# Kernel optimization log

Hardware: AMD Instinct MI355X
Metric: run time of the kernel (lower is better)

The kernel has to match this reference:

```python
import jax, jax.numpy as jnp
import numpy as np

B, L = 16, 1024
D_MODEL, D_STATE, N_LAYERS = 256, 16, 2
FRAME_DIM, N_FRAMES, N_ACT = 115, 4, 19
GNN_H, GNN_K, ACT_EMB, GRID, N_PLAYERS = 32, 6, 16, 5, 22


def _ln(x, g, b, eps=1e-5):
    m = x.mean(-1, keepdims=True)
    v = ((x - m) ** 2).mean(-1, keepdims=True)
    return (x - m) / jnp.sqrt(v + eps) * g + b


def _kan(x, g, b, Wsp, Wbase, bias, beta):
    # x: [N, FRAME_DIM]
    grid = jnp.linspace(-1.0, 1.0, GRID)
    x = _ln(x, g, b)
    bta = jnp.clip(beta, 0.5, 6.0)
    basis = jnp.exp(-((x[..., None] - grid) ** 2) * bta)  # [N, I, G]
    # original: einsum('bdig,oid->bod').sum(-1) with basis dim d==1 broadcast
    # == sum over i, g (basis) and d (spline grid axis)
    spline = jnp.einsum('big,oid->bo', basis, Wsp)
    base = x @ Wbase.T
    return base + spline + bias


def _graph(fc, fp):
    # fc, fp: [N, 115] current / previous frame
    Bn = fc.shape[0]
    ball = fc[:, :2]
    lp = fc[:, 3:25].reshape(Bn, 11, 2)
    rp = fc[:, 25:47].reshape(Bn, 11, 2)
    lpp = fp[:, 3:25].reshape(Bn, 11, 2)
    rpp = fp[:, 25:47].reshape(Bn, 11, 2)
    pos = jnp.concatenate([lp, rp], 1)           # [N, 22, 2]
    posp = jnp.concatenate([lpp, rpp], 1)
    vel = pos - posp
    team = jnp.concatenate([jnp.zeros((Bn, 11, 1)), jnp.ones((Bn, 11, 1))], 1)
    bd = jnp.sqrt(((pos - ball[:, None, :]) ** 2).sum(-1, keepdims=True))
    prox = jnp.exp(-bd * 2)
    lc = lp.mean(1, keepdims=True)
    rc = rp.mean(1, keepdims=True)
    tc = jnp.concatenate([jnp.broadcast_to(lc, (Bn, 11, 2)),
                          jnp.broadcast_to(rc, (Bn, 11, 2))], 1)
    nodes = jnp.concatenate([pos, vel, team, prox, pos - tc], -1)  # [N, 22, 8]
    eye = jnp.eye(N_PLAYERS)
    d = jnp.sqrt(((pos[:, :, None, :] - pos[:, None, :, :]) ** 2).sum(-1)) + eye * 1e6
    _, idx = jax.lax.top_k(-d, GNN_K)
    adj = jax.nn.one_hot(idx, N_PLAYERS).sum(-2)
    adj = jnp.minimum(adj + eye, 1.0)
    adj = adj / jnp.clip(adj.sum(-1, keepdims=True), 1.0, None)
    # the torch model computes the graph under no_grad
    return jax.lax.stop_gradient(nodes), jax.lax.stop_gradient(adj)


def _s6(x, h0, lng, lnb, Win, Wdt, bdt, Alog, WB, WC, Dp, Wout):
    Bn, Ln, Dm = x.shape
    h0 = h0.reshape(Bn, Dm, D_STATE)
    xn = _ln(x, lng, lnb)
    xz = xn @ Win.T
    x_in, z = jnp.split(xz, 2, axis=-1)
    dt = jax.nn.softplus(x_in @ Wdt.T + bdt)     # [B, L, D]
    A = -jnp.exp(Alog)                            # [D, N]
    Bt = x_in @ WB.T                              # [B, L, N]
    Ct = x_in @ WC.T

    def step(h, inp):
        dt_t, x_t, B_t, C_t = inp                 # [B,D],[B,D],[B,N],[B,N]
        dA = jnp.exp(dt_t[:, :, None] * A)        # [B, D, N]
        h = dA * h + (dt_t * x_t)[:, :, None] * B_t[:, None, :]
        y = (h * C_t[:, None, :]).sum(-1)         # [B, D]
        return h, y

    hL, ys = jax.lax.scan(step, h0, (dt.swapaxes(0, 1), x_in.swapaxes(0, 1),
                                     Bt.swapaxes(0, 1), Ct.swapaxes(0, 1)))
    y = ys.swapaxes(0, 1)
    ssm = y * jax.nn.silu(z) + x_in * Dp
    return x + ssm @ Wout.T, hL.reshape(Bn, -1)


def setup_inputs() -> dict:
    key = jax.random.key(0)
    ks = iter(jax.random.split(key, 80))

    def nrm(shape, s=0.05):
        return jax.random.normal(next(ks), shape, dtype=jnp.float32) * s

    inp = {}
    inp['obs'] = jax.random.normal(next(ks), (B, L, N_FRAMES, FRAME_DIM), dtype=jnp.float32)
    inp['prev_actions'] = jax.random.randint(next(ks), (B, L), 0, N_ACT)
    inp['h0_0'] = jnp.zeros((B, D_MODEL * D_STATE), jnp.float32)
    inp['h0_1'] = jnp.zeros((B, D_MODEL * D_STATE), jnp.float32)
    inp['kan_ln_g'] = jnp.ones((FRAME_DIM,), jnp.float32)
    inp['kan_ln_b'] = jnp.zeros((FRAME_DIM,), jnp.float32)
    inp['kan_spline'] = nrm((D_MODEL, FRAME_DIM, GRID), 0.1)
    inp['kan_scale'] = jnp.ones((D_MODEL, FRAME_DIM), jnp.float32)
    inp['kan_bias'] = jnp.zeros((D_MODEL,), jnp.float32)
    inp['kan_beta'] = jnp.full((1,), 2.0, jnp.float32)
    inp['fn_g'] = jnp.ones((D_MODEL,), jnp.float32)
    inp['fn_b'] = jnp.zeros((D_MODEL,), jnp.float32)
    inp['gnn_W'] = nrm((GNN_H, 8))
    inp['edge_w'] = jnp.full((1,), 0.5, jnp.float32)
    inp['act_emb'] = nrm((N_ACT, ACT_EMB), 1.0)
    inp['W_ip'] = nrm((D_MODEL, D_MODEL + GNN_H + ACT_EMB))
    inp['b_ip'] = jnp.zeros((D_MODEL,), jnp.float32)
    for i in range(N_LAYERS):
        p = 'm%d_' % i
        inp[p + 'lng'] = jnp.ones((D_MODEL,), jnp.float32)
        inp[p + 'lnb'] = jnp.zeros((D_MODEL,), jnp.float32)
        inp[p + 'Win'] = nrm((2 * D_MODEL, D_MODEL))
        inp[p + 'Wdt'] = nrm((D_MODEL, D_MODEL))
        inp[p + 'bdt'] = jnp.zeros((D_MODEL,), jnp.float32)
        inp[p + 'Alog'] = jax.random.uniform(next(ks), (D_MODEL, D_STATE),
                                             minval=-3.0, maxval=-1.0, dtype=jnp.float32)
        inp[p + 'WB'] = nrm((D_STATE, D_MODEL))
        inp[p + 'WC'] = nrm((D_STATE, D_MODEL))
        inp[p + 'D'] = jnp.ones((D_MODEL,), jnp.float32)
        inp[p + 'Wout'] = nrm((D_MODEL, D_MODEL))
    inp['fl_g'] = jnp.ones((D_MODEL,), jnp.float32)
    inp['fl_b'] = jnp.zeros((D_MODEL,), jnp.float32)
    inp['pW1'] = nrm((128, D_MODEL)); inp['pb1'] = jnp.zeros((128,), jnp.float32)
    inp['pW2'] = nrm((N_ACT, 128)); inp['pb2'] = jnp.zeros((N_ACT,), jnp.float32)
    inp['vW1'] = nrm((64, D_MODEL)); inp['vb1'] = jnp.zeros((64,), jnp.float32)
    inp['vW2'] = nrm((1, 64)); inp['vb2'] = jnp.zeros((1,), jnp.float32)
    return inp


def reference(obs, prev_actions, h0_0, h0_1,
              kan_ln_g, kan_ln_b, kan_spline, kan_scale, kan_bias, kan_beta,
              fn_g, fn_b, gnn_W, edge_w, act_emb, W_ip, b_ip,
              m0_lng, m0_lnb, m0_Win, m0_Wdt, m0_bdt, m0_Alog, m0_WB, m0_WC, m0_D, m0_Wout,
              m1_lng, m1_lnb, m1_Win, m1_Wdt, m1_bdt, m1_Alog, m1_WB, m1_WC, m1_D, m1_Wout,
              fl_g, fl_b, pW1, pb1, pW2, pb2, vW1, vb1, vW2, vb2):
    BL = B * L
    # frame encoder (KAN) over all frames of all timesteps
    flat = obs.reshape(BL * N_FRAMES, FRAME_DIM)
    fe = _kan(flat, kan_ln_g, kan_ln_b, kan_spline, kan_scale, kan_bias, kan_beta)
    fe = jax.nn.relu(_ln(fe.reshape(BL, N_FRAMES, D_MODEL), fn_g, fn_b))
    feat = fe.mean(1)                                   # [BL, D]
    # GNN on last two frames
    fc = obs[:, :, -1, :].reshape(BL, FRAME_DIM)
    fp = obs[:, :, -2, :].reshape(BL, FRAME_DIM)
    nodes, adj = _graph(fc, fp)
    gx = nodes @ gnn_W.T                                # [BL, 22, H]
    agg = jnp.einsum('bij,bjd->bid', adj, gx)
    gx = gx * (1 - edge_w) + agg * edge_w
    gemb = gx.mean(1)                                   # [BL, H]
    aemb = act_emb[prev_actions].reshape(BL, ACT_EMB)
    x = jnp.concatenate([feat, gemb, aemb], -1) @ W_ip.T + b_ip
    x = x.reshape(B, L, D_MODEL)
    x, h1 = _s6(x, h0_0, m0_lng, m0_lnb, m0_Win, m0_Wdt, m0_bdt, m0_Alog, m0_WB, m0_WC, m0_D, m0_Wout)
    x, h2 = _s6(x, h0_1, m1_lng, m1_lnb, m1_Win, m1_Wdt, m1_bdt, m1_Alog, m1_WB, m1_WC, m1_D, m1_Wout)
    x = _ln(x, fl_g, fl_b)
    logits = jax.nn.relu(x @ pW1.T + pb1) @ pW2.T + pb2   # [B, L, N_ACT]
    value = (jax.nn.relu(x @ vW1.T + vb1) @ vW2.T + vb2)[..., 0]  # [B, L]
    return logits, value, h1, h2
```

## Files before the change

### kernel.cpp

```cpp
#include <hip/hip_runtime.h>
#include <math.h>

#define BB   16
#define LL   1024
#define BLR  (BB*LL)
#define DM   256
#define DS   16
#define FD   115
#define NF   4
#define NACTN 19
#define GH   32
#define GKN  6
#define AEM  16
#define NP   22
#define CATD 304
#define CATP 320
#define KKANP 256
#define KREALK 230
#define NC   16
#define CL   (LL/NC)
#define TT   16
#define LDK  40
#define XZW  800


typedef __attribute__((ext_vector_type(8))) short bf16x8;
typedef __attribute__((ext_vector_type(4))) float f32x4;

__device__ inline unsigned short f2bf(float f) {
    unsigned int u = __float_as_uint(f);
    u += 0x7fff + ((u >> 16) & 1);
    return (unsigned short)(u >> 16);
}
__device__ inline unsigned int f2bf2(float lo, float hi) {
    return (unsigned int)f2bf(lo) | ((unsigned int)f2bf(hi) << 16);
}
__device__ inline size_t swz(int row, int k) {
    return (size_t)(row >> 4)*4096 + (k >> 5)*512 + ((k >> 3) & 3)*128
         + (row & 15)*8 + (k & 7);
}

template<int NFRAG>
__global__ __launch_bounds__(256) void bgemm(
    const unsigned short* __restrict__ A, const unsigned short* __restrict__ W,
    const float* __restrict__ bias, float* __restrict__ C,
    int ldc, int act, int accum)
{
    const int tid = threadIdx.x;
    const int wid = tid >> 6, lane = tid & 63;
    const int wr = wid >> 1, wc = wid & 1;
    const int g = lane >> 4, r16 = lane & 15;
    const int bm = blockIdx.x * 64;
    const int bn = blockIdx.y * (NFRAG * 32);

    f32x4 acc[2][NFRAG] = {};
    const unsigned short* abase = A + ((size_t)(bm >> 4) + wr*2)*4096 + g*128 + r16*8;
    const unsigned short* wbase = W + ((size_t)(bn >> 4) + wc*NFRAG)*4096 + g*128 + r16*8;
    #pragma unroll
    for (int kk = 0; kk < 8; ++kk) {
        bf16x8 a0 = *(const bf16x8*)(abase + kk*512);
        bf16x8 a1 = *(const bf16x8*)(abase + 4096 + kk*512);
        bf16x8 bfr[NFRAG];
        #pragma unroll
        for (int ni = 0; ni < NFRAG; ++ni)
            bfr[ni] = *(const bf16x8*)(wbase + (size_t)ni*4096 + kk*512);
        #pragma unroll
        for (int ni = 0; ni < NFRAG; ++ni) {
            acc[0][ni] = __builtin_amdgcn_mfma_f32_16x16x32_bf16(a0, bfr[ni], acc[0][ni], 0,0,0);
            acc[1][ni] = __builtin_amdgcn_mfma_f32_16x16x32_bf16(a1, bfr[ni], acc[1][ni], 0,0,0);
        }
    }
    #pragma unroll
    for (int mi = 0; mi < 2; ++mi) {
        #pragma unroll
        for (int j = 0; j < 4; ++j) {
            int row = bm + wr*32 + mi*16 + g*4 + j;
            float* crow = C + (size_t)row * ldc;
            #pragma unroll
            for (int ni = 0; ni < NFRAG; ++ni) {
                int col = bn + wc*(NFRAG*16) + ni*16 + r16;
                float v = acc[mi][ni][j];
                if (act == 3) {
                    if (col >= 512 && col < 768) {
                        v += bias[col - 512];
                        v = fmaxf(v, 0.f) + __logf(1.f + __expf(-fabsf(v)));
                    }
                } else {
                    if (bias) v += bias[col];
                    if (act == 1) v = fmaxf(v, 0.f);
                }
                if (accum) v += crow[col];
                crow[col] = v;
            }
        }
    }
}

__global__ __launch_bounds__(256) void mfma_gemm(
    const float* __restrict__ A, const unsigned short* __restrict__ W,
    const float* __restrict__ bias, float* __restrict__ C,
    int N, int Kp, int Kreal, int lda, int ldc, int act, int accum)
{
    __shared__ __align__(16) unsigned short As[128*LDK];
    __shared__ __align__(16) unsigned short Ws[128*LDK];
    const int tid = threadIdx.x;
    const int bm = blockIdx.x * 128;
    const int bn = blockIdx.y * 128;
    const int wid = tid >> 6, lane = tid & 63;
    const int wr = wid >> 1, wc = wid & 1;
    const int g = lane >> 4, r16 = lane & 15;
    const int srow = tid >> 1;
    const int shalf = (tid & 1) * 16;

    f32x4 acc[4][4] = {};
    for (int k0 = 0; k0 < Kp; k0 += 32) {
        uint4 alo = make_uint4(0u,0u,0u,0u), ahi = make_uint4(0u,0u,0u,0u);
        if (k0 + shalf < Kreal) {
            const float* ap = A + (size_t)(bm + srow) * lda + k0 + shalf;
            float4 a0 = *(const float4*)(ap);
            float4 a1 = *(const float4*)(ap + 4);
            float4 a2 = *(const float4*)(ap + 8);
            float4 a3 = *(const float4*)(ap + 12);
            alo = make_uint4(f2bf2(a0.x,a0.y), f2bf2(a0.z,a0.w),
                             f2bf2(a1.x,a1.y), f2bf2(a1.z,a1.w));
            ahi = make_uint4(f2bf2(a2.x,a2.y), f2bf2(a2.z,a2.w),
                             f2bf2(a3.x,a3.y), f2bf2(a3.z,a3.w));
        }
        unsigned short* ad = &As[srow*LDK + shalf];
        *(uint4*)(ad)     = alo;
        *(uint4*)(ad + 8) = ahi;
        int n = bn + srow;
        uint4 wv0 = make_uint4(0u,0u,0u,0u), wv1 = make_uint4(0u,0u,0u,0u);
        if (n < N) {
            const unsigned short* wp = W + (size_t)n * Kp + k0 + shalf;
            wv0 = ((const uint4*)wp)[0];
            wv1 = ((const uint4*)wp)[1];
        }
        unsigned short* wd = &Ws[srow*LDK + shalf];
        *(uint4*)(wd)     = wv0;
        *(uint4*)(wd + 8) = wv1;
        __syncthreads();

        bf16x8 af[4], bfr[4];
        #pragma unroll
        for (int mi = 0; mi < 4; ++mi)
            af[mi] = *reinterpret_cast<const bf16x8*>(&As[(wr*64 + mi*16 + r16)*LDK + g*8]);
        #pragma unroll
        for (int ni = 0; ni < 4; ++ni)
            bfr[ni] = *reinterpret_cast<const bf16x8*>(&Ws[(wc*64 + ni*16 + r16)*LDK + g*8]);
        #pragma unroll
        for (int mi = 0; mi < 4; ++mi)
            #pragma unroll
            for (int ni = 0; ni < 4; ++ni)
                acc[mi][ni] = __builtin_amdgcn_mfma_f32_16x16x32_bf16(
                    af[mi], bfr[ni], acc[mi][ni], 0, 0, 0);
        __syncthreads();
    }
    #pragma unroll
    for (int mi = 0; mi < 4; ++mi) {
        #pragma unroll
        for (int j = 0; j < 4; ++j) {
            int row = bm + wr*64 + mi*16 + g*4 + j;
            float* crow = C + (size_t)row * ldc;
            #pragma unroll
            for (int ni = 0; ni < 4; ++ni) {
                int col = bn + wc*64 + ni*16 + r16;
                if (col < N) {
                    float v = acc[mi][ni][j];
                    if (bias) v += bias[col];
                    if (act == 1) v = fmaxf(v, 0.f);
                    if (accum) v += crow[col];
                    crow[col] = v;
                }
            }
        }
    }
}

__global__ __launch_bounds__(256) void kan_statgen(
    const float* __restrict__ obs, const float* __restrict__ lng,
    const float* __restrict__ lnb, const float* __restrict__ betap,
    unsigned short* __restrict__ AG)
{
    int row = blockIdx.x * 4 + (threadIdx.x >> 6);
    int l = threadIdx.x & 63;
    const float beta = fminf(fmaxf(betap[0], 0.5f), 6.0f);
    const float* o = obs + (size_t)row * FD;
    float v0 = o[l];
    float v1 = (l + 64 < FD) ? o[l + 64] : 0.f;
    float s = v0 + v1;
    for (int off = 32; off; off >>= 1) s += __shfl_xor(s, off);
    float m = s * (1.f / FD);
    float e0 = v0 - m;
    float e1 = (l + 64 < FD) ? (v1 - m) : 0.f;
    float ss = e0*e0 + e1*e1;
    for (int off = 32; off; off >>= 1) ss += __shfl_xor(ss, off);
    float rs = rsqrtf(ss * (1.f / FD) + 1e-5f);

    float x0 = e0 * rs * lng[l] + lnb[l];
    float sb0 = 0.f;
    #pragma unroll
    for (int g5 = 0; g5 < 5; ++g5) {
        float dx = x0 - (-1.f + 0.5f * (float)g5);
        sb0 += __expf(-dx*dx*beta);
    }
    unsigned int u0 = f2bf2(x0, sb0);
    unsigned int u1 = 0u;
    if (l + 64 < FD) {
        float x1 = e1 * rs * lng[l+64] + lnb[l+64];
        float sb1 = 0.f;
        #pragma unroll
        for (int g5 = 0; g5 < 5; ++g5) {
            float dx = x1 - (-1.f + 0.5f * (float)g5);
            sb1 += __expf(-dx*dx*beta);
        }
        u1 = f2bf2(x1, sb1);
    }
    size_t base = (size_t)(row >> 4) * 4096 + (row & 15) * 8
                + ((l >> 2) & 3) * 128 + ((2*l) & 7);
    *(unsigned int*)(AG + base + ((l >> 4)    ) * 512) = u0;
    *(unsigned int*)(AG + base + ((l >> 4) + 4) * 512) = u1;
}

__global__ void prep_wf16(const float* __restrict__ sp, const float* __restrict__ sc,
                          unsigned short* __restrict__ Wg)
{
    int idx = blockIdx.x * 256 + threadIdx.x;
    if (idx >= DM * KKANP) return;
    int o = idx >> 8, k = idx & 255;
    float v = 0.f;
    if (k < KREALK) {
        int i = k >> 1;
        if (k & 1) {
            const float* s5 = sp + ((size_t)o*FD + i)*5;
            v = s5[0] + s5[1] + s5[2] + s5[3] + s5[4];
        } else v = sc[o*FD + i];
    }
    Wg[swz(o, k)] = f2bf(v);
}

__global__ __launch_bounds__(256) void kan_gemm2(
    const unsigned short* __restrict__ AG, const unsigned short* __restrict__ WF,
    const float* __restrict__ kbias, const float* __restrict__ fng,
    const float* __restrict__ fnb, float* __restrict__ cat)
{
    __shared__ float rsum[64][2];
    __shared__ float rsq[64][2];
    const int tid = threadIdx.x;
    const int bm = blockIdx.x * 64;
    const int wid = tid >> 6, lane = tid & 63;
    const int wr = wid >> 1, wc = wid & 1;
    const int g = lane >> 4, r16 = lane & 15;

    f32x4 acc[2][8] = {};
    const unsigned short* abase = AG + ((size_t)(bm >> 4) + wr*2)*4096 + g*128 + r16*8;
    const unsigned short* wbase = WF + (size_t)(wc*8)*4096 + g*128 + r16*8;
    #pragma unroll
    for (int kk = 0; kk < 8; ++kk) {
        bf16x8 af0 = *(const bf16x8*)(abase + kk*512);
        bf16x8 af1 = *(const bf16x8*)(abase + 4096 + kk*512);
        bf16x8 bfr[8];
        #pragma unroll
        for (int ni = 0; ni < 8; ++ni)
            bfr[ni] = *(const bf16x8*)(wbase + (size_t)ni*4096 + kk*512);
        #pragma unroll
        for (int ni = 0; ni < 8; ++ni) {
            acc[0][ni] = __builtin_amdgcn_mfma_f32_16x16x32_bf16(af0, bfr[ni], acc[0][ni], 0,0,0);
            acc[1][ni] = __builtin_amdgcn_mfma_f32_16x16x32_bf16(af1, bfr[ni], acc[1][ni], 0,0,0);
        }
    }
    float bias8[8], g8[8], b8[8];
    #pragma unroll
    for (int ni = 0; ni < 8; ++ni) {
        int col = wc*128 + ni*16 + r16;
        bias8[ni] = kbias[col]; g8[ni] = fng[col]; b8[ni] = fnb[col];
    }
    #pragma unroll
    for (int mi = 0; mi < 2; ++mi) {
        #pragma unroll
        for (int j = 0; j < 4; ++j) {
            float s = 0.f, q = 0.f;
            #pragma unroll
            for (int ni = 0; ni < 8; ++ni) {
                float v = acc[mi][ni][j] + bias8[ni];
                s += v; q += v*v;
            }
            #pragma unroll
            for (int off = 1; off < 16; off <<= 1) {
                s += __shfl_xor(s, off);
                q += __shfl_xor(q, off);
            }
            if (r16 == 0) {
                int row = wr*32 + mi*16 + g*4 + j;
                rsum[row][wc] = s; rsq[row][wc] = q;
            }
        }
    }
    __syncthreads();
    #pragma unroll
    for (int mi = 0; mi < 2; ++mi) {
        int row0 = wr*32 + mi*16 + g*4;
        float o8[8] = {0.f,0.f,0.f,0.f,0.f,0.f,0.f,0.f};
        #pragma unroll
        for (int j = 0; j < 4; ++j) {
            int row = row0 + j;
            float sm = rsum[row][0] + rsum[row][1];
            float sq = rsq[row][0] + rsq[row][1];
            float mn = sm * (1.f/256.f);
            float var = fmaxf(sq * (1.f/256.f) - mn*mn, 0.f);
            float rstd = rsqrtf(var + 1e-5f);
            #pragma unroll
            for (int ni = 0; ni < 8; ++ni) {
                float v = acc[mi][ni][j] + bias8[ni];
                v = (v - mn) * rstd * g8[ni] + b8[ni];
                o8[ni] += fmaxf(v, 0.f);
            }
        }
        int rbl = (bm + row0) >> 2;
        float* crow = cat + (size_t)rbl * CATD;
        #pragma unroll
        for (int ni = 0; ni < 8; ++ni)
            crow[wc*128 + ni*16 + r16] = o8[ni] * 0.25f;
    }
}

__global__ __launch_bounds__(256) void gemm_f32(
    const float* __restrict__ A, const float* __restrict__ W,
    const float* __restrict__ bias, float* __restrict__ C,
    int N, int K, int lda, int ldc, int act, int accum)
{
    __shared__ float As[16][68];
    __shared__ float Ws[16][68];
    const int tid = threadIdx.x;
    const int bm = blockIdx.x * 64;
    const int bn = blockIdx.y * 64;
    const int ty = tid >> 4, tx = tid & 15;
    const int lr = tid >> 2;
    const int lk = (tid & 3) * 4;
    float acc[4][4] = {{0.f,0.f,0.f,0.f},{0.f,0.f,0.f,0.f},{0.f,0.f,0.f,0.f},{0.f,0.f,0.f,0.f}};

    for (int k0 = 0; k0 < K; k0 += 16) {
        float4 av = *reinterpret_cast<const float4*>(A + (size_t)(bm + lr) * lda + k0 + lk);
        As[lk+0][lr] = av.x; As[lk+1][lr] = av.y; As[lk+2][lr] = av.z; As[lk+3][lr] = av.w;
        float4 wv = make_float4(0.f, 0.f, 0.f, 0.f);
        if (bn + lr < N)
            wv = *reinterpret_cast<const float4*>(W + (size_t)(bn + lr) * K + k0 + lk);
        Ws[lk+0][lr] = wv.x; Ws[lk+1][lr] = wv.y; Ws[lk+2][lr] = wv.z; Ws[lk+3][lr] = wv.w;
        __syncthreads();
        #pragma unroll
        for (int kk = 0; kk < 16; ++kk) {
            float4 a4 = *reinterpret_cast<const float4*>(&As[kk][ty*4]);
            float4 b4 = *reinterpret_cast<const float4*>(&Ws[kk][tx*4]);
            float aa[4] = {a4.x, a4.y, a4.z, a4.w};
            float bb[4] = {b4.x, b4.y, b4.z, b4.w};
            #pragma unroll
            for (int i = 0; i < 4; ++i)
                #pragma unroll
                for (int j = 0; j < 4; ++j)
                    acc[i][j] = fmaf(aa[i], bb[j], acc[i][j]);
        }
        __syncthreads();
    }
    #pragma unroll
    for (int i = 0; i < 4; ++i) {
        int row = bm + ty*4 + i;
        #pragma unroll
        for (int j = 0; j < 4; ++j) {
            int col = bn + tx*4 + j;
            if (col < N) {
                float v = acc[i][j];
                if (bias) v += bias[col];
                if (act == 1) v = fmaxf(v, 0.f);
                size_t o = (size_t)row * ldc + col;
                if (accum) v += C[o];
                C[o] = v;
            }
        }
    }
}

__global__ void prep_bf16(const float* __restrict__ src, unsigned short* __restrict__ dst,
                          int N, int K, int Kp)
{
    int idx = blockIdx.x * 256 + threadIdx.x;
    if (idx >= N * Kp) return;
    int n = idx / Kp, k = idx - n * Kp;
    dst[idx] = (k < K) ? f2bf(src[(size_t)n * K + k]) : (unsigned short)0;
}

__global__ void prep_bf16_swz(const float* __restrict__ src,
                              unsigned short* __restrict__ dst, int N)
{
    int idx = blockIdx.x * 256 + threadIdx.x;
    if (idx >= N * DM) return;
    int n = idx >> 8, k = idx & 255;
    dst[swz(n, k)] = f2bf(src[idx]);
}

__global__ void prep_layerw(
    const float* __restrict__ Win, const float* __restrict__ WB,
    const float* __restrict__ WC, const float* __restrict__ Wdt,
    const float* __restrict__ Wout,
    unsigned short* __restrict__ WINX16, unsigned short* __restrict__ WOUT16)
{
    int idx = blockIdx.x * 256 + threadIdx.x;
    if (idx < 512*256) {
        int n = idx >> 8, k = idx & 255;
        WINX16[swz(n, k)] = f2bf(Win[idx]);
    } else if (idx < 768*256) {
        int j2 = idx - 512*256;
        int n = j2 >> 8, k = j2 & 255;
        const float* src = Wdt + (size_t)n*DM;
        float acc = 0.f;
        for (int j = 0; j < DM; ++j)
            acc = fmaf(src[j], Win[(size_t)j*DM + k], acc);
        WINX16[swz(512 + n, k)] = f2bf(acc);
    } else if (idx < 800*256) {
        int j2 = idx - 768*256;
        int n = j2 >> 8, k = j2 & 255;
        const float* src = (n < 16) ? (WB + n*DM) : (WC + (n-16)*DM);
        float acc = 0.f;
        for (int j = 0; j < DM; ++j)
            acc = fmaf(src[j], Win[(size_t)j*DM + k], acc);
        WINX16[swz(768 + n, k)] = f2bf(acc);
    } else if (idx < 800*256 + 256*256) {
        int j2 = idx - 800*256;
        int n = j2 >> 8, k = j2 & 255;
        WOUT16[swz(n, k)] = f2bf(Wout[j2]);
    }
}

__global__ __launch_bounds__(64) void graph_kernel(const float* __restrict__ obs,
    const float* __restrict__ gW, const float* __restrict__ ewp,
    float* __restrict__ out)
{
    __shared__ float px[NP], py[NP];
    __shared__ float nodes[NP][8];
    __shared__ float gxs[NP][GH];
    __shared__ unsigned int msk[NP];
    __shared__ float rden[NP];
    __shared__ float wgt[NP];
    const int row = blockIdx.x;
    const int lane = threadIdx.x;
    const float* fc = obs + ((size_t)row * NF + 3) * FD;
    const float* fp = obs + ((size_t)row * NF + 2) * FD;
    const float ew = ewp[0];

    if (lane < NP) {
        int i = lane;
        float p0, p1, q0, q1;
        if (i < 11) { p0 = fc[3+2*i];  p1 = fc[4+2*i];  q0 = fp[3+2*i];  q1 = fp[4+2*i]; }
        else { int ii = i-11; p0 = fc[25+2*ii]; p1 = fc[26+2*ii]; q0 = fp[25+2*ii]; q1 = fp[26+2*ii]; }
        px[i] = p0; py[i] = p1;
        float bx = fc[0], by = fc[1];
        float bd = sqrtf((p0-bx)*(p0-bx) + (p1-by)*(p1-by));
        nodes[i][0] = p0; nodes[i][1] = p1;
        nodes[i][2] = p0 - q0; nodes[i][3] = p1 - q1;
        nodes[i][4] = (i < 11) ? 0.f : 1.f;
        nodes[i][5] = __expf(-2.f * bd);
    }
    __syncthreads();
    if (lane < NP) {
        int base = (lane < 11) ? 0 : 11;
        float cx = 0.f, cy = 0.f;
        for (int j = 0; j < 11; ++j) { cx += px[base+j]; cy += py[base+j]; }
        cx *= (1.f/11.f); cy *= (1.f/11.f);
        nodes[lane][6] = px[lane] - cx;
        nodes[lane][7] = py[lane] - cy;
        unsigned sel = 0;
        for (int k = 0; k < GKN; ++k) {
            float best = 1e30f; int bj = 0;
            for (int j = 0; j < NP; ++j) {
                if (j == lane || ((sel >> j) & 1u)) continue;
                float dx = px[lane]-px[j], dy = py[lane]-py[j];
                float dd = sqrtf(dx*dx + dy*dy);
                if (dd < best) { best = dd; bj = j; }
            }
            sel |= (1u << bj);
        }
        unsigned full = sel | (1u << lane);
        msk[lane] = full;
        rden[lane] = 1.f / fmaxf((float)__popc(full), 1.f);
    }
    __syncthreads();
    for (int idx = lane; idx < NP*GH; idx += 64) {
        int i = idx >> 5, h = idx & 31;
        float s = 0.f;
        #pragma unroll
        for (int f = 0; f < 8; ++f) s += nodes[i][f] * gW[h*8 + f];
        gxs[i][h] = s;
    }
    __syncthreads();
    if (lane < NP) {
        float s = 0.f;
        for (int i = 0; i < NP; ++i) if ((msk[i] >> lane) & 1u) s += rden[i];
        wgt[lane] = (1.f - ew) + ew * s;
    }
    __syncthreads();
    if (lane < GH) {
        float s = 0.f;
        for (int j = 0; j < NP; ++j) s += wgt[j] * gxs[j][lane];
        out[(size_t)row * CATD + DM + lane] = s * (1.f/22.f);
    }
}

__global__ void gather_aemb(const int* __restrict__ pa, const float* __restrict__ emb,
                            float* __restrict__ out)
{
    int idx = blockIdx.x * 256 + threadIdx.x;
    int row = idx >> 4, e = idx & 15;
    out[(size_t)row * CATD + DM + GH + e] = emb[pa[row]*AEM + e];
}

__global__ __launch_bounds__(256) void ln256_swz(const float* __restrict__ X,
    const float* __restrict__ g, const float* __restrict__ b,
    unsigned short* __restrict__ Y16)
{
    int row = blockIdx.x * 4 + (threadIdx.x >> 6);
    int lane = threadIdx.x & 63;
    const float* x = X + (size_t)row * DM;
    float4 v = reinterpret_cast<const float4*>(x)[lane];
    float s = v.x + v.y + v.z + v.w;
    for (int off = 32; off; off >>= 1) s += __shfl_xor(s, off);
    float m = s * (1.f / DM);
    float d0 = v.x-m, d1 = v.y-m, d2 = v.z-m, d3 = v.w-m;
    float ss = d0*d0 + d1*d1 + d2*d2 + d3*d3;
    for (int off = 32; off; off >>= 1) ss += __shfl_xor(ss, off);
    float rstd = rsqrtf(ss * (1.f / DM) + 1e-5f);
    int c = lane * 4;
    float o0 = d0*rstd*g[c+0] + b[c+0];
    float o1 = d1*rstd*g[c+1] + b[c+1];
    float o2 = d2*rstd*g[c+2] + b[c+2];
    float o3 = d3*rstd*g[c+3] + b[c+3];
    size_t base = swz(row, c);
    *(uint2*)(Y16 + base) = make_uint2(f2bf2(o0, o1), f2bf2(o2, o3));
}

__global__ __launch_bounds__(256) void s6_chunkA(
    const float* __restrict__ xz, const float* __restrict__ Alog,
    float* __restrict__ P, float* __restrict__ S)
{
    __shared__ float sdt[TT][64], sx[TT][64];
    __shared__ __align__(16) float sB[TT][16];
    const int blk = blockIdx.x;
    const int dblk = blk & 3, c = (blk >> 2) & 15, b = blk >> 6;
    const int sg = threadIdx.x & 3, dl = threadIdx.x >> 2;
    const int d0 = dblk*64, d = d0 + dl;
    float A[4];
    #pragma unroll
    for (int k = 0; k < 4; ++k) A[k] = -__expf(Alog[d*DS + sg*4 + k]);
    const size_t r0 = (size_t)b*LL + c*CL;
    const int lt = threadIdx.x >> 4, lc = (threadIdx.x & 15) * 4;
    float Pv[4] = {1.f,1.f,1.f,1.f}, Sv[4] = {0.f,0.f,0.f,0.f};
    for (int t0 = 0; t0 < CL; t0 += TT) {
        size_t rb = r0 + t0 + lt;
        *(float4*)&sdt[lt][lc] = *(const float4*)(xz + rb*XZW + 512 + d0 + lc);
        *(float4*)&sx[lt][lc]  = *(const float4*)(xz + rb*XZW + d0 + lc);
        if (threadIdx.x < 64) {
            size_t rb2 = r0 + t0 + (threadIdx.x >> 2);
            *(float4*)&sB[threadIdx.x >> 2][(threadIdx.x & 3)*4] =
                *(const float4*)(xz + rb2*XZW + 768 + (threadIdx.x & 3)*4);
        }
        __syncthreads();
        #pragma unroll
        for (int tt = 0; tt < TT; ++tt) {
            float dtv = sdt[tt][dl];
            float u   = dtv * sx[tt][dl];
            float4 Bv = *(const float4*)&sB[tt][sg*4];
            float bb[4] = {Bv.x, Bv.y, Bv.z, Bv.w};
            #pragma unroll
            for (int k = 0; k < 4; ++k) {
                float dA = __expf(dtv * A[k]);
                Pv[k] *= dA;
                Sv[k] = fmaf(dA, Sv[k], u * bb[k]);
            }
        }
        __syncthreads();
    }
    size_t o = (((size_t)b*NC + c)*DM + d)*DS + sg*4;
    *(float4*)(P + o) = make_float4(Pv[0], Pv[1], Pv[2], Pv[3]);
    *(float4*)(S + o) = make_float4(Sv[0], Sv[1], Sv[2], Sv[3]);
}

__global__ __launch_bounds__(256) void s6_comb(
    const float* __restrict__ P, const float* __restrict__ S,
    const float* __restrict__ h0, float* __restrict__ hin, float* __restrict__ hout)
{
    int idx = blockIdx.x * 256 + threadIdx.x;
    int b = idx >> 12, ds = idx & 4095;
    float h = h0[idx];
    #pragma unroll
    for (int c = 0; c < NC; ++c) {
        size_t o = (((size_t)b*NC + c) << 12) + ds;
        hin[o] = h;
        h = fmaf(P[o], h, S[o]);
    }
    hout[idx] = h;
}

__global__ __launch_bounds__(256) void s6_chunkC(
    const float* __restrict__ xz, const float* __restrict__ Alog,
    const float* __restrict__ hin, const float* __restrict__ Dp,
    unsigned short* __restrict__ ssm16)
{
    __shared__ float sdt[TT][64], sx[TT][64], sz[TT][64];
    __shared__ __align__(16) float sB[TT][16], sC[TT][16];
    const int blk = blockIdx.x;
    const int dblk = blk & 3, c = (blk >> 2) & 15, b = blk >> 6;
    const int sg = threadIdx.x & 3, dl = threadIdx.x >> 2;
    const int d0 = dblk*64, d = d0 + dl;
    float A[4];
    #pragma unroll
    for (int k = 0; k < 4; ++k) A[k] = -__expf(Alog[d*DS + sg*4 + k]);
    const float Dv = Dp[d];
    const size_t r0 = (size_t)b*LL + c*CL;
    const int lt = threadIdx.x >> 4, lc = (threadIdx.x & 15) * 4;
    float4 h4 = *(const float4*)(hin + (((size_t)b*NC + c)*DM + d)*DS + sg*4);
    float h[4] = {h4.x, h4.y, h4.z, h4.w};
    for (int t0 = 0; t0 < CL; t0 += TT) {
        size_t rb = r0 + t0 + lt;
        *(float4*)&sdt[lt][lc] = *(const float4*)(xz + rb*XZW + 512 + d0 + lc);
        *(float4*)&sx[lt][lc]  = *(const float4*)(xz + rb*XZW + d0 + lc);
        *(float4*)&sz[lt][lc]  = *(const float4*)(xz + rb*XZW + 256 + d0 + lc);
        if (threadIdx.x < 128) {
            size_t rb2 = r0 + t0 + ((threadIdx.x & 63) >> 2);
            int col = (threadIdx.x & 3) * 4;
            if (threadIdx.x < 64)
                *(float4*)&sB[(threadIdx.x & 63) >> 2][col] =
                    *(const float4*)(xz + rb2*XZW + 768 + col);
            else
                *(float4*)&sC[(threadIdx.x & 63) >> 2][col] =
                    *(const float4*)(xz + rb2*XZW + 784 + col);
        }
        __syncthreads();
        #pragma unroll
        for (int tt = 0; tt < TT; ++tt) {
            float dtv = sdt[tt][dl];
            float xv  = sx[tt][dl];
            float u   = dtv * xv;
            float4 Bv = *(const float4*)&sB[tt][sg*4];
            float4 Cv = *(const float4*)&sC[tt][sg*4];
            float bb[4] = {Bv.x, Bv.y, Bv.z, Bv.w};
            float cc[4] = {Cv.x, Cv.y, Cv.z, Cv.w};
            float p = 0.f;
            #pragma unroll
            for (int k = 0; k < 4; ++k) {
                float dA = __expf(dtv * A[k]);
                h[k] = fmaf(dA, h[k], u * bb[k]);
                p = fmaf(h[k], cc[k], p);
            }
            p += __shfl_xor(p, 1);
            p += __shfl_xor(p, 2);
            if (sg == 0) {
                float zv = sz[tt][dl];
                float sil = zv / (1.f + __expf(-zv));
                int row = (int)(r0 + t0 + tt);
                ssm16[swz(row, d)] = f2bf(fmaf(p, sil, xv * Dv));
            }
        }
        __syncthreads();
    }
}

static inline void mgemm(hipStream_t st, const float* A, const unsigned short* W,
                         const float* bias, float* C, int M, int N, int Kp, int Kreal,
                         int lda, int ldc, int act, int accum) {
    dim3 g(M/128, (N+127)/128);
    mfma_gemm<<<g, 256, 0, st>>>(A, W, bias, C, N, Kp, Kreal, lda, ldc, act, accum);
}
static inline void gemm(hipStream_t st, const float* A, const float* W, const float* bias,
                        float* C, int M, int N, int K, int lda, int ldc, int act, int accum) {
    dim3 g(M/64, (N+63)/64);
    gemm_f32<<<g, 256, 0, st>>>(A, W, bias, C, N, K, lda, ldc, act, accum);
}

extern "C" void kernel_launch(void* const* d_in, const int* in_sizes, int n_in,
                              void* d_out, int out_size, void* d_ws, size_t ws_size,
                              hipStream_t stream) {
    (void)in_sizes; (void)n_in; (void)out_size; (void)ws_size;
    const float* obs      = (const float*)d_in[0];
    const int*   pa       = (const int*)d_in[1];
    const float* h0in[2]  = {(const float*)d_in[2], (const float*)d_in[3]};
    const float* kan_ln_g = (const float*)d_in[4];
    const float* kan_ln_b = (const float*)d_in[5];
    const float* kan_sp   = (const float*)d_in[6];
    const float* kan_sc   = (const float*)d_in[7];
    const float* kan_bias = (const float*)d_in[8];
    const float* kan_beta = (const float*)d_in[9];
    const float* fn_g     = (const float*)d_in[10];
    const float* fn_b     = (const float*)d_in[11];
    const float* gnn_W    = (const float*)d_in[12];
    const float* edge_w   = (const float*)d_in[13];
    const float* act_emb  = (const float*)d_in[14];
    const float* W_ip     = (const float*)d_in[15];
    const float* b_ip     = (const float*)d_in[16];
    const float* fl_g     = (const float*)d_in[37];
    const float* fl_b     = (const float*)d_in[38];
    const float* pW1      = (const float*)d_in[39];
    const float* pb1      = (const float*)d_in[40];
    const float* pW2      = (const float*)d_in[41];
    const float* pb2      = (const float*)d_in[42];
    const float* vW1      = (const float*)d_in[43];
    const float* vb1      = (const float*)d_in[44];
    const float* vW2      = (const float*)d_in[45];
    const float* vb2      = (const float*)d_in[46];

    const size_t SZ_BIG = (size_t)BLR * DM;
    float* ws = (float*)d_ws;
    float* X    = ws;
    float* R0   = X + SZ_BIG;
    unsigned short* XN16  = (unsigned short*)R0;
    unsigned short* SSM16 = XN16 + (size_t)BLR*DM;
    unsigned short* WIP16 = (unsigned short*)R0;
    unsigned short* WF16  = WIP16 + (size_t)DM*CATP;
    float* XZBC = R0 + SZ_BIG;
    unsigned short* AG16 = (unsigned short*)XZBC;
    float* R4   = XZBC + (size_t)BLR * XZW;
    const size_t CH = (size_t)BB * NC * DM * DS;
    float* Pbuf = R4;
    float* Sbuf = R4 + CH;
    float* HIN  = R4 + 2*CH;
    unsigned short* WINX16[2];
    WINX16[0] = (unsigned short*)(R4 + 3*CH);
    WINX16[1] = WINX16[0] + (size_t)XZW*DM;
    unsigned short* WOUT16[2];
    WOUT16[0] = WINX16[1] + (size_t)XZW*DM;
    WOUT16[1] = WOUT16[0] + DM*DM;
    unsigned short* PW116 = WOUT16[1] + DM*DM;
    unsigned short* VW116 = PW116 + 128*DM;

    float* out        = (float*)d_out;
    float* out_logits = out;
    float* out_value  = out + (size_t)BLR * NACTN;
    float* out_h[2]   = {out + (size_t)BLR*NACTN + BLR,
                         out + (size_t)BLR*NACTN + BLR + (size_t)BB*DM*DS};

    prep_wf16<<<(DM*KKANP+255)/256, 256, 0, stream>>>(kan_sp, kan_sc, WF16);
    prep_bf16<<<(DM*CATP+255)/256, 256, 0, stream>>>(W_ip, WIP16, DM, CATD, CATP);
    kan_statgen<<<BLR*NF/4, 256, 0, stream>>>(obs, kan_ln_g, kan_ln_b, kan_beta, AG16);
    kan_gemm2<<<BLR*NF/64, 256, 0, stream>>>(AG16, WF16, kan_bias, fn_g, fn_b, R4);
    graph_kernel<<<BLR, 64, 0, stream>>>(obs, gnn_W, edge_w, R4);
    gather_aemb<<<BLR*AEM/256, 256, 0, stream>>>(pa, act_emb, R4);

    mgemm(stream, R4, WIP16, b_ip, X, BLR, DM, CATP, CATD, CATD, DM, 0, 0);

    prep_bf16_swz<<<(128*DM+255)/256, 256, 0, stream>>>(pW1, PW116, 128);
    prep_bf16_swz<<<(64*DM+255)/256, 256, 0, stream>>>(vW1, VW116, 64);
    for (int l = 0; l < 2; ++l) {
        const float* Win  = (const float*)d_in[17 + 10*l + 2];
        const float* Wdt  = (const float*)d_in[17 + 10*l + 3];
        const float* WBp  = (const float*)d_in[17 + 10*l + 6];
        const float* WCp  = (const float*)d_in[17 + 10*l + 7];
        const float* Wout = (const float*)d_in[17 + 10*l + 9];
        prep_layerw<<<(800*256 + 256*256 + 255)/256, 256, 0, stream>>>(
            Win, WBp, WCp, Wdt, Wout, WINX16[l], WOUT16[l]);
    }

    for (int l = 0; l < 2; ++l) {
        const float* lng  = (const float*)d_in[17 + 10*l + 0];
        const float* lnb  = (const float*)d_in[17 + 10*l + 1];
        const float* bdt  = (const float*)d_in[17 + 10*l + 4];
        const float* Alog = (const float*)d_in[17 + 10*l + 5];
        const float* Dp   = (const float*)d_in[17 + 10*l + 8];

        ln256_swz<<<BLR/4, 256, 0, stream>>>(X, lng, lnb, XN16);
        bgemm<5><<<dim3(BLR/64, 5), 256, 0, stream>>>(
            XN16, WINX16[l], bdt, XZBC, XZW, 3, 0);
        s6_chunkA<<<BB*NC*4, 256, 0, stream>>>(XZBC, Alog, Pbuf, Sbuf);
        s6_comb<<<BB*DM*DS/256, 256, 0, stream>>>(Pbuf, Sbuf, h0in[l], HIN, out_h[l]);
        s6_chunkC<<<BB*NC*4, 256, 0, stream>>>(XZBC, Alog, HIN, Dp, SSM16);
        bgemm<4><<<dim3(BLR/64, 2), 256, 0, stream>>>(
            SSM16, WOUT16[l], nullptr, X, DM, 0, 1);
    }

    float* H1 = XZBC;
    float* H2 = XZBC + (size_t)BLR*128;
    ln256_swz<<<BLR/4, 256, 0, stream>>>(X, fl_g, fl_b, XN16);
    bgemm<4><<<dim3(BLR/64, 1), 256, 0, stream>>>(XN16, PW116, pb1, H1, 128, 1, 0);
    gemm(stream, H1, pW2, pb2, out_logits, BLR, NACTN, 128, 128, NACTN, 0, 0);
    bgemm<2><<<dim3(BLR/64, 1), 256, 0, stream>>>(XN16, VW116, vb1, H2, 64, 1, 0);
    gemm(stream, H2, vW2, vb2, out_value, BLR, 1, 64, 64, 1, 0, 0);
}
```

Measured before the change: 389.0 us.

## Fuse layernorm into out-projection epilogue and merge policy/value head GEMMs

Replaces the out-projection GEMM plus separate layernorm with a single kernel. It adds the residual, computes row statistics across the tile, and writes the normalized bf16 input for the next layer or head. The policy and value first-layer weights are concatenated into one GEMM. The action-embedding gather is folded into a graph kernel that now processes four rows per block. This removes several full passes over the activation buffer and some launches, at the cost of a one-pass variance formula and a higher register load in the fused epilogue.

```diff
diff --git a/kernel.cpp b/kernel.cpp
--- a/kernel.cpp
+++ b/kernel.cpp
@@ -96,6 +96,90 @@
     }
 }
 
+__global__ __launch_bounds__(256) void bgemm_ln(
+    const unsigned short* __restrict__ A, const unsigned short* __restrict__ W,
+    float* __restrict__ X, const float* __restrict__ g8p,
+    const float* __restrict__ b8p, unsigned short* __restrict__ Y16)
+{
+    __shared__ float rsum[64][2];
+    __shared__ float rsq[64][2];
+    const int tid = threadIdx.x;
+    const int bm = blockIdx.x * 64;
+    const int wid = tid >> 6, lane = tid & 63;
+    const int wr = wid >> 1, wc = wid & 1;
+    const int g = lane >> 4, r16 = lane & 15;
+
+    f32x4 acc[2][8] = {};
+    const unsigned short* abase = A + ((size_t)(bm >> 4) + wr*2)*4096 + g*128 + r16*8;
+    const unsigned short* wbase = W + (size_t)(wc*8)*4096 + g*128 + r16*8;
+    #pragma unroll
+    for (int kk = 0; kk < 8; ++kk) {
+        bf16x8 a0 = *(const bf16x8*)(abase + kk*512);
+        bf16x8 a1 = *(const bf16x8*)(abase + 4096 + kk*512);
+        bf16x8 bfr[8];
+        #pragma unroll
+        for (int ni = 0; ni < 8; ++ni)
+            bfr[ni] = *(const bf16x8*)(wbase + (size_t)ni*4096 + kk*512);
+        #pragma unroll
+        for (int ni = 0; ni < 8; ++ni) {
+            acc[0][ni] = __builtin_amdgcn_mfma_f32_16x16x32_bf16(a0, bfr[ni], acc[0][ni], 0,0,0);
+            acc[1][ni] = __builtin_amdgcn_mfma_f32_16x16x32_bf16(a1, bfr[ni], acc[1][ni], 0,0,0);
+        }
+    }
+    #pragma unroll
+    for (int mi = 0; mi < 2; ++mi) {
+        #pragma unroll
+        for (int j = 0; j < 4; ++j) {
+            int row = bm + wr*32 + mi*16 + g*4 + j;
+            float* xrow = X + (size_t)row * DM;
+            float s = 0.f, q = 0.f;
+            #pragma unroll
+            for (int ni = 0; ni < 8; ++ni) {
+                int col = wc*128 + ni*16 + r16;
+                float v = acc[mi][ni][j] + xrow[col];
+                acc[mi][ni][j] = v;
+                xrow[col] = v;
+                s += v; q += v*v;
+            }
+            #pragma unroll
+            for (int off = 1; off < 16; off <<= 1) {
+                s += __shfl_xor(s, off);
+                q += __shfl_xor(q, off);
+            }
+            if (r16 == 0) {
+                int lrow = wr*32 + mi*16 + g*4 + j;
+                rsum[lrow][wc] = s; rsq[lrow][wc] = q;
+            }
+        }
+    }
+    __syncthreads();
+    float g8[8], b8[8];
+    #pragma unroll
+    for (int ni = 0; ni < 8; ++ni) {
+        int col = wc*128 + ni*16 + r16;
+        g8[ni] = g8p[col]; b8[ni] = b8p[col];
+    }
+    #pragma unroll
+    for (int mi = 0; mi < 2; ++mi) {
+        #pragma unroll
+        for (int j = 0; j < 4; ++j) {
+            int lrow = wr*32 + mi*16 + g*4 + j;
+            int row = bm + lrow;
+            float sm = rsum[lrow][0] + rsum[lrow][1];
+            float sq = rsq[lrow][0] + rsq[lrow][1];
+            float mn = sm * (1.f/256.f);
+            float var = fmaxf(sq * (1.f/256.f) - mn*mn, 0.f);
+            float rstd = rsqrtf(var + 1e-5f);
+            #pragma unroll
+            for (int ni = 0; ni < 8; ++ni) {
+                int col = wc*128 + ni*16 + r16;
+                float v = (acc[mi][ni][j] - mn) * rstd * g8[ni] + b8[ni];
+                Y16[swz(row, col)] = f2bf(v);
+            }
+        }
+    }
+}
+
 __global__ __launch_bounds__(256) void mfma_gemm(
     const float* __restrict__ A, const unsigned short* __restrict__ W,
     const float* __restrict__ bias, float* __restrict__ C,
@@ -168,7 +252,6 @@
                 if (col < N) {
                     float v = acc[mi][ni][j];
                     if (bias) v += bias[col];
-                    if (act == 1) v = fmaxf(v, 0.f);
                     if (accum) v += crow[col];
                     crow[col] = v;
                 }
@@ -388,13 +471,19 @@
     dst[idx] = (k < K) ? f2bf(src[(size_t)n * K + k]) : (unsigned short)0;
 }
 
-__global__ void prep_bf16_swz(const float* __restrict__ src,
-                              unsigned short* __restrict__ dst, int N)
+__global__ void prep_pv(const float* __restrict__ pW1, const float* __restrict__ vW1,
+                        const float* __restrict__ pb1, const float* __restrict__ vb1,
+                        unsigned short* __restrict__ PV16, float* __restrict__ PVB)
 {
     int idx = blockIdx.x * 256 + threadIdx.x;
-    if (idx >= N * DM) return;
-    int n = idx >> 8, k = idx & 255;
-    dst[swz(n, k)] = f2bf(src[idx]);
+    if (idx < 192*256) {
+        int n = idx >> 8, k = idx & 255;
+        float v = (n < 128) ? pW1[(size_t)n*DM + k] : vW1[(size_t)(n-128)*DM + k];
+        PV16[swz(n, k)] = f2bf(v);
+    } else if (idx < 192*256 + 192) {
+        int i = idx - 192*256;
+        PVB[i] = (i < 128) ? pb1[i] : vb1[i-128];
+    }
 }
 
 __global__ void prep_layerw(
@@ -430,18 +519,20 @@
     }
 }
 
-__global__ __launch_bounds__(64) void graph_kernel(const float* __restrict__ obs,
+__global__ __launch_bounds__(256) void graph_kernel4(const float* __restrict__ obs,
     const float* __restrict__ gW, const float* __restrict__ ewp,
+    const int* __restrict__ pa, const float* __restrict__ emb,
     float* __restrict__ out)
 {
-    __shared__ float px[NP], py[NP];
-    __shared__ float nodes[NP][8];
-    __shared__ float gxs[NP][GH];
-    __shared__ unsigned int msk[NP];
-    __shared__ float rden[NP];
-    __shared__ float wgt[NP];
-    const int row = blockIdx.x;
-    const int lane = threadIdx.x;
+    __shared__ float px[4][NP], py[4][NP];
+    __shared__ float nodes[4][NP][8];
+    __shared__ float gxs[4][NP][GH];
+    __shared__ unsigned int msk[4][NP];
+    __shared__ float rden[4][NP];
+    __shared__ float wgt[4][NP];
+    const int w = threadIdx.x >> 6;
+    const int lane = threadIdx.x & 63;
+    const int row = blockIdx.x * 4 + w;
     const float* fc = obs + ((size_t)row * NF + 3) * FD;
     const float* fp = obs + ((size_t)row * NF + 2) * FD;
     const float ew = ewp[0];
@@ -451,65 +542,60 @@
         float p0, p1, q0, q1;
         if (i < 11) { p0 = fc[3+2*i];  p1 = fc[4+2*i];  q0 = fp[3+2*i];  q1 = fp[4+2*i]; }
         else { int ii = i-11; p0 = fc[25+2*ii]; p1 = fc[26+2*ii]; q0 = fp[25+2*ii]; q1 = fp[26+2*ii]; }
-        px[i] = p0; py[i] = p1;
+        px[w][i] = p0; py[w][i] = p1;
         float bx = fc[0], by = fc[1];
         float bd = sqrtf((p0-bx)*(p0-bx) + (p1-by)*(p1-by));
-        nodes[i][0] = p0; nodes[i][1] = p1;
-        nodes[i][2] = p0 - q0; nodes[i][3] = p1 - q1;
-        nodes[i][4] = (i < 11) ? 0.f : 1.f;
-        nodes[i][5] = __expf(-2.f * bd);
+        nodes[w][i][0] = p0; nodes[w][i][1] = p1;
+        nodes[w][i][2] = p0 - q0; nodes[w][i][3] = p1 - q1;
+        nodes[w][i][4] = (i < 11) ? 0.f : 1.f;
+        nodes[w][i][5] = __expf(-2.f * bd);
+    } else if (lane >= 32 && lane < 32 + AEM) {
+        int e = lane - 32;
+        out[(size_t)row * CATD + DM + GH + e] = emb[pa[row]*AEM + e];
     }
     __syncthreads();
     if (lane < NP) {
         int base = (lane < 11) ? 0 : 11;
         float cx = 0.f, cy = 0.f;
-        for (int j = 0; j < 11; ++j) { cx += px[base+j]; cy += py[base+j]; }
+        for (int j = 0; j < 11; ++j) { cx += px[w][base+j]; cy += py[w][base+j]; }
         cx *= (1.f/11.f); cy *= (1.f/11.f);
-        nodes[lane][6] = px[lane] - cx;
-        nodes[lane][7] = py[lane] - cy;
+        nodes[w][lane][6] = px[w][lane] - cx;
+        nodes[w][lane][7] = py[w][lane] - cy;
         unsigned sel = 0;
         for (int k = 0; k < GKN; ++k) {
             float best = 1e30f; int bj = 0;
             for (int j = 0; j < NP; ++j) {
                 if (j == lane || ((sel >> j) & 1u)) continue;
-                float dx = px[lane]-px[j], dy = py[lane]-py[j];
+                float dx = px[w][lane]-px[w][j], dy = py[w][lane]-py[w][j];
                 float dd = sqrtf(dx*dx + dy*dy);
                 if (dd < best) { best = dd; bj = j; }
             }
             sel |= (1u << bj);
         }
         unsigned full = sel | (1u << lane);
-        msk[lane] = full;
-        rden[lane] = 1.f / fmaxf((float)__popc(full), 1.f);
+        msk[w][lane] = full;
+        rden[w][lane] = 1.f / fmaxf((float)__popc(full), 1.f);
     }
     __syncthreads();
     for (int idx = lane; idx < NP*GH; idx += 64) {
         int i = idx >> 5, h = idx & 31;
         float s = 0.f;
         #pragma unroll
-        for (int f = 0; f < 8; ++f) s += nodes[i][f] * gW[h*8 + f];
-        gxs[i][h] = s;
+        for (int f = 0; f < 8; ++f) s += nodes[w][i][f] * gW[h*8 + f];
+        gxs[w][i][h] = s;
     }
     __syncthreads();
     if (lane < NP) {
         float s = 0.f;
-        for (int i = 0; i < NP; ++i) if ((msk[i] >> lane) & 1u) s += rden[i];
-        wgt[lane] = (1.f - ew) + ew * s;
+        for (int i = 0; i < NP; ++i) if ((msk[w][i] >> lane) & 1u) s += rden[w][i];
+        wgt[w][lane] = (1.f - ew) + ew * s;
     }
     __syncthreads();
     if (lane < GH) {
         float s = 0.f;
-        for (int j = 0; j < NP; ++j) s += wgt[j] * gxs[j][lane];
+        for (int j = 0; j < NP; ++j) s += wgt[w][j] * gxs[w][j][lane];
         out[(size_t)row * CATD + DM + lane] = s * (1.f/22.f);
     }
-}
-
-__global__ void gather_aemb(const int* __restrict__ pa, const float* __restrict__ emb,
-                            float* __restrict__ out)
-{
-    int idx = blockIdx.x * 256 + threadIdx.x;
-    int row = idx >> 4, e = idx & 15;
-    out[(size_t)row * CATD + DM + GH + e] = emb[pa[row]*AEM + e];
 }
 
 __global__ __launch_bounds__(256) void ln256_swz(const float* __restrict__ X,
@@ -726,8 +812,8 @@
     unsigned short* WOUT16[2];
     WOUT16[0] = WINX16[1] + (size_t)XZW*DM;
     WOUT16[1] = WOUT16[0] + DM*DM;
-    unsigned short* PW116 = WOUT16[1] + DM*DM;
-    unsigned short* VW116 = PW116 + 128*DM;
+    unsigned short* PV16 = WOUT16[1] + DM*DM;
+    float* PVB = (float*)(PV16 + 192*DM);
 
     float* out        = (float*)d_out;
     float* out_logits = out;
@@ -739,13 +825,11 @@
     prep_bf16<<<(DM*CATP+255)/256, 256, 0, stream>>>(W_ip, WIP16, DM, CATD, CATP);
     kan_statgen<<<BLR*NF/4, 256, 0, stream>>>(obs, kan_ln_g, kan_ln_b, kan_beta, AG16);
     kan_gemm2<<<BLR*NF/64, 256, 0, stream>>>(AG16, WF16, kan_bias, fn_g, fn_b, R4);
-    graph_kernel<<<BLR, 64, 0, stream>>>(obs, gnn_W, edge_w, R4);
-    gather_aemb<<<BLR*AEM/256, 256, 0, stream>>>(pa, act_emb, R4);
+    graph_kernel4<<<BLR/4, 256, 0, stream>>>(obs, gnn_W, edge_w, pa, act_emb, R4);
 
     mgemm(stream, R4, WIP16, b_ip, X, BLR, DM, CATP, CATD, CATD, DM, 0, 0);
 
-    prep_bf16_swz<<<(128*DM+255)/256, 256, 0, stream>>>(pW1, PW116, 128);
-    prep_bf16_swz<<<(64*DM+255)/256, 256, 0, stream>>>(vW1, VW116, 64);
+    prep_pv<<<(192*256 + 192 + 255)/256, 256, 0, stream>>>(pW1, vW1, pb1, vb1, PV16, PVB);
     for (int l = 0; l < 2; ++l) {
         const float* Win  = (const float*)d_in[17 + 10*l + 2];
         const float* Wdt  = (const float*)d_in[17 + 10*l + 3];
@@ -756,28 +840,25 @@
             Win, WBp, WCp, Wdt, Wout, WINX16[l], WOUT16[l]);
     }
 
+    ln256_swz<<<BLR/4, 256, 0, stream>>>(X, (const float*)d_in[17], (const float*)d_in[18], XN16);
+
     for (int l = 0; l < 2; ++l) {
-        const float* lng  = (const float*)d_in[17 + 10*l + 0];
-        const float* lnb  = (const float*)d_in[17 + 10*l + 1];
         const float* bdt  = (const float*)d_in[17 + 10*l + 4];
         const float* Alog = (const float*)d_in[17 + 10*l + 5];
         const float* Dp   = (const float*)d_in[17 + 10*l + 8];
-
-        ln256_swz<<<BLR/4, 256, 0, stream>>>(X, lng, lnb, XN16);
+        const float* nlg  = (l == 0) ? (const float*)d_in[27] : fl_g;
+        const float* nlb  = (l == 0) ? (const float*)d_in[28] : fl_b;
+
         bgemm<5><<<dim3(BLR/64, 5), 256, 0, stream>>>(
             XN16, WINX16[l], bdt, XZBC, XZW, 3, 0);
         s6_chunkA<<<BB*NC*4, 256, 0, stream>>>(XZBC, Alog, Pbuf, Sbuf);
         s6_comb<<<BB*DM*DS/256, 256, 0, stream>>>(Pbuf, Sbuf, h0in[l], HIN, out_h[l]);
         s6_chunkC<<<BB*NC*4, 256, 0, stream>>>(XZBC, Alog, HIN, Dp, SSM16);
-        bgemm<4><<<dim3(BLR/64, 2), 256, 0, stream>>>(
-            SSM16, WOUT16[l], nullptr, X, DM, 0, 1);
-    }
-
-    float* H1 = XZBC;
-    float* H2 = XZBC + (size_t)BLR*128;
-    ln256_swz<<<BLR/4, 256, 0, stream>>>(X, fl_g, fl_b, XN16);
-    bgemm<4><<<dim3(BLR/64, 1), 256, 0, stream>>>(XN16, PW116, pb1, H1, 128, 1, 0);
-    gemm(stream, H1, pW2, pb2, out_logits, BLR, NACTN, 128, 128, NACTN, 0, 0);
-    bgemm<2><<<dim3(BLR/64, 1), 256, 0, stream>>>(XN16, VW116, vb1, H2, 64, 1, 0);
-    gemm(stream, H2, vW2, vb2, out_value, BLR, 1, 64, 64, 1, 0, 0);
-}
+        bgemm_ln<<<BLR/64, 256, 0, stream>>>(SSM16, WOUT16[l], X, nlg, nlb, XN16);
+    }
+
+    float* H = XZBC;
+    bgemm<6><<<dim3(BLR/64, 1), 256, 0, stream>>>(XN16, PV16, PVB, H, 192, 1, 0);
+    gemm(stream, H, pW2, pb2, out_logits, BLR, NACTN, 128, 192, NACTN, 0, 0);
+    gemm(stream, H + 128, vW2, vb2, out_value, BLR, 1, 64, 192, 1, 0, 0);
+}
```

Result: slower. 418.9 us (+7.7%).
